# Optimization experiments

Measured on AMD Instinct MI355X. Metric: run time of the kernel, lower is better.

## Reference

```python
import jax, jax.numpy as jnp
import numpy as np

N_SRNA = 20000
N_MRNA = 100000
HID = 128
E_S2M = 1_000_000
E_M2M = 2_000_000
E_LBL = 500_000
N_LAYERS = 2


def setup_inputs() -> dict:
    key = jax.random.key(0)
    ks = jax.random.split(key, 20)
    s = 0.05
    inp = {
        # edge lists (rev edge types are flips, derived inside reference)
        "s2m_src": jax.random.randint(ks[0], (E_S2M,), 0, N_SRNA),
        "s2m_dst": jax.random.randint(ks[1], (E_S2M,), 0, N_MRNA),
        "m2m_src": jax.random.randint(ks[2], (E_M2M,), 0, N_MRNA),
        "m2m_dst": jax.random.randint(ks[3], (E_M2M,), 0, N_MRNA),
        "label_src": jax.random.randint(ks[4], (E_LBL,), 0, N_SRNA),
        "label_dst": jax.random.randint(ks[5], (E_LBL,), 0, N_MRNA),
        # embeddings (node_id is arange over all nodes -> identity lookup)
        "srna_emb": jax.random.normal(ks[6], (N_SRNA, HID), jnp.float32),
        "mrna_emb": jax.random.normal(ks[7], (N_MRNA, HID), jnp.float32),
        # per-layer stacked params. SAGEConv: out = lin_l(mean_agg)+lin_r(x_dst)
        "sage_s2m_Wl": jax.random.normal(ks[8], (N_LAYERS, HID, HID), jnp.float32) * s,
        "sage_s2m_bl": jnp.zeros((N_LAYERS, HID), jnp.float32),
        "sage_s2m_Wr": jax.random.normal(ks[9], (N_LAYERS, HID, HID), jnp.float32) * s,
        "sage_rev_Wl": jax.random.normal(ks[10], (N_LAYERS, HID, HID), jnp.float32) * s,
        "sage_rev_bl": jnp.zeros((N_LAYERS, HID), jnp.float32),
        "sage_rev_Wr": jax.random.normal(ks[11], (N_LAYERS, HID, HID), jnp.float32) * s,
        # GCNConv: out = propagate(norm, x @ W) + b
        "gcn_m2m_W": jax.random.normal(ks[12], (N_LAYERS, HID, HID), jnp.float32) * s,
        "gcn_m2m_b": jnp.zeros((N_LAYERS, HID), jnp.float32),
        "gcn_rev_W": jax.random.normal(ks[13], (N_LAYERS, HID, HID), jnp.float32) * s,
        "gcn_rev_b": jnp.zeros((N_LAYERS, HID), jnp.float32),
    }
    return inp


def _sage(x_src, x_dst, src, dst, n_dst, Wl, bl, Wr):
    # PyG SAGEConv (aggr='mean', root_weight=True): lin_l(mean_msg) + lin_r(x_dst)
    agg = jax.ops.segment_sum(x_src[src], dst, num_segments=n_dst)  # [n_dst, h]
    cnt = jax.ops.segment_sum(jnp.ones((src.shape[0],), x_src.dtype), dst,
                              num_segments=n_dst)
    agg = agg / jnp.maximum(cnt, 1.0)[:, None]
    return agg @ Wl + bl + x_dst @ Wr


def _gcn(x, src, dst, n, W, b):
    # PyG GCNConv: add self-loops, sym-normalize, x @ W, propagate, + bias
    xw = x @ W  # [n, h]
    deg = jax.ops.segment_sum(jnp.ones((src.shape[0],), x.dtype), dst,
                              num_segments=n) + 1.0  # +1 self-loop
    dinv = jax.lax.rsqrt(deg)
    norm = dinv[src] * dinv[dst]  # [E]
    out = jax.ops.segment_sum(norm[:, None] * xw[src], dst, num_segments=n)
    out = out + (dinv * dinv)[:, None] * xw  # self-loop term
    return out + b


def reference(s2m_src, s2m_dst, m2m_src, m2m_dst, label_src, label_dst,
              srna_emb, mrna_emb,
              sage_s2m_Wl, sage_s2m_bl, sage_s2m_Wr,
              sage_rev_Wl, sage_rev_bl, sage_rev_Wr,
              gcn_m2m_W, gcn_m2m_b, gcn_rev_W, gcn_rev_b):
    x_s, x_m = srna_emb, mrna_emb
    for l in range(N_LAYERS):
        # HeteroConv aggr='sum' over edge types per dst node type
        m_new = _sage(x_s, x_m, s2m_src, s2m_dst, N_MRNA,
                      sage_s2m_Wl[l], sage_s2m_bl[l], sage_s2m_Wr[l])
        m_new = m_new + _gcn(x_m, m2m_src, m2m_dst, N_MRNA,
                             gcn_m2m_W[l], gcn_m2m_b[l])
        m_new = m_new + _gcn(x_m, m2m_dst, m2m_src, N_MRNA,
                             gcn_rev_W[l], gcn_rev_b[l])  # rev_similar = flip
        s_new = _sage(x_m, x_s, s2m_dst, s2m_src, N_SRNA,
                      sage_rev_Wl[l], sage_rev_bl[l], sage_rev_Wr[l])
        x_s, x_m = jax.nn.relu(s_new), jax.nn.relu(m_new)
    # Classifier: dot product over labeled (srna, mrna) pairs
    return (x_s[label_src] * x_m[label_dst]).sum(axis=-1)
```

## Files before the change

### kernel.cpp

```cpp
#include <hip/hip_runtime.h>
#include <hip/hip_fp16.h>

#define NS 20000
#define NM 100000
#define H  128
#define ES 1000000
#define EM 2000000
#define EL 500000

#define SH_M 7
#define SH_S 6
#define NB_SD 782
#define NB_SS 313
#define NB_MD 782
#define NB_MS 782
#define CAP_SD 1664
#define CAP_SS 3904
#define CAP_MD 3200
#define CAP_MS 3200
#define MAXCAP 3904
#define CHUNK 4096
#define B_SD ((ES + CHUNK - 1) / CHUNK)
#define B_SS ((ES + CHUNK - 1) / CHUNK)
#define B_MD ((EM + CHUNK - 1) / CHUNK)
#define B_MS ((EM + CHUNK - 1) / CHUNK)
#define VAL_MASK 0x1FFFF

typedef _Float16 half8 __attribute__((ext_vector_type(8)));
typedef float floatx4 __attribute__((ext_vector_type(4)));

__global__ __launch_bounds__(256) void place1_sorted(
        const int* __restrict__ s2m_src, const int* __restrict__ s2m_dst,
        const int* __restrict__ m2m_src, const int* __restrict__ m2m_dst,
        int* __restrict__ bc,
        unsigned int* __restrict__ p_sd, unsigned int* __restrict__ p_ss,
        unsigned int* __restrict__ p_md, unsigned int* __restrict__ p_ms) {
    __shared__ unsigned int rec[CHUNK];
    __shared__ unsigned short eb[CHUNK];
    __shared__ int cnt[1024];
    __shared__ int gbase[1024];

    int b = blockIdx.x;
    const int *keys, *vals; int shift, cap, E, bcoff; unsigned int* pp;
    int cb;
    if (b < B_SD)                    { cb = b;                      keys = s2m_dst; vals = s2m_src; shift = SH_M; cap = CAP_SD; E = ES; bcoff = 0;     pp = p_sd; }
    else if (b < B_SD+B_SS)          { cb = b - B_SD;               keys = s2m_src; vals = s2m_dst; shift = SH_S; cap = CAP_SS; E = ES; bcoff = 16384; pp = p_ss; }
    else if (b < B_SD+B_SS+B_MD)     { cb = b - B_SD - B_SS;        keys = m2m_dst; vals = m2m_src; shift = SH_M; cap = CAP_MD; E = EM; bcoff = 32768; pp = p_md; }
    else                             { cb = b - B_SD - B_SS - B_MD; keys = m2m_src; vals = m2m_dst; shift = SH_M; cap = CAP_MS; E = EM; bcoff = 49152; pp = p_ms; }
    int* bcp = bc + bcoff;

    int t = threadIdx.x;
    int e0 = cb * CHUNK;
    int nv = E - e0; if (nv > CHUNK) nv = CHUNK;

    for (int i = t; i < nv; i += 256) {
        int k = keys[e0 + i];
        int v = vals[e0 + i];
        int bkt = k >> shift;
        rec[i] = ((unsigned int)(k - (bkt << shift)) << 17) | (unsigned int)v;
        eb[i] = (unsigned short)bkt;
    }
#pragma unroll
    for (int j = 0; j < 4; ++j) cnt[t * 4 + j] = 0;
    __syncthreads();
    for (int i = t; i < nv; i += 256) atomicAdd(&cnt[eb[i]], 1);
    __syncthreads();
#pragma unroll
    for (int j = 0; j < 4; ++j) {
        int bk = t * 4 + j;
        int c = cnt[bk];
        if (c > 0) {
            gbase[bk] = atomicAdd(&bcp[bk << 4], c);
            cnt[bk] = 0;
        }
    }
    __syncthreads();
    for (int i = t; i < nv; i += 256) {
        int bk = eb[i];
        int pos = atomicAdd(&cnt[bk], 1);
        int o = gbase[bk] + pos;
        if (o < cap) pp[(size_t)bk * cap + o] = rec[i];
    }
}

__global__ __launch_bounds__(256) void place2_fused(
        const int* __restrict__ bc,
        const unsigned int* __restrict__ p_sd, const unsigned int* __restrict__ p_ss,
        const unsigned int* __restrict__ p_md, const unsigned int* __restrict__ p_ms,
        int* __restrict__ adj_sd, int* __restrict__ adj_ss,
        int* __restrict__ adj_md, int* __restrict__ adj_ms,
        int* __restrict__ off_sd, int* __restrict__ off_ss,
        int* __restrict__ off_md, int* __restrict__ off_ms,
        int* __restrict__ cnt_sd, int* __restrict__ cnt_ss,
        int* __restrict__ cnt_md, int* __restrict__ cnt_ms) {
    __shared__ unsigned int lp[MAXCAP];
    __shared__ int hist[128], cur[128], sbuf[128];
    int b = blockIdx.x;
    int c, lb;
    if (b < NB_SD)                    { c = 0; lb = b; }
    else if (b < NB_SD+NB_SS)         { c = 1; lb = b - NB_SD; }
    else if (b < NB_SD+NB_SS+NB_MD)   { c = 2; lb = b - NB_SD - NB_SS; }
    else                              { c = 3; lb = b - NB_SD - NB_SS - NB_MD; }
    const unsigned int* pp; int *adj, *offp, *cntp; int shift, cap, n;
    switch (c) {
    case 0:  pp = p_sd; adj = adj_sd; offp = off_sd; cntp = cnt_sd; shift = SH_M; cap = CAP_SD; n = NM; break;
    case 1:  pp = p_ss; adj = adj_ss; offp = off_ss; cntp = cnt_ss; shift = SH_S; cap = CAP_SS; n = NS; break;
    case 2:  pp = p_md; adj = adj_md; offp = off_md; cntp = cnt_md; shift = SH_M; cap = CAP_MD; n = NM; break;
    default: pp = p_ms; adj = adj_ms; offp = off_ms; cntp = cnt_ms; shift = SH_M; cap = CAP_MS; n = NM; break;
    }
    int t = threadIdx.x;
    int k = bc[c * 16384 + (lb << 4)];
    if (k > cap) k = cap;
    int base = lb << shift;
    int npb = 1 << shift;
    int bb = lb * cap;
    for (int i = t; i < k; i += 256) lp[i] = pp[(size_t)lb * cap + i];
    if (t < npb) hist[t] = 0;
    __syncthreads();
    for (int i = t; i < k; i += 256) atomicAdd(&hist[lp[i] >> 17], 1);
    __syncthreads();
    int v = (t < npb) ? hist[t] : 0;
    if (t < 128) sbuf[t] = v;
    __syncthreads();
    for (int d = 1; d < 128; d <<= 1) {
        int x = 0;
        if (t >= d && t < 128) x = sbuf[t - d];
        __syncthreads();
        if (t >= d && t < 128) sbuf[t] += x;
        __syncthreads();
    }
    if (t < npb) {
        int excl = sbuf[t] - v;
        cur[t] = excl;
        int node = base + t;
        if (node < n) { offp[node] = bb + excl; cntp[node] = v; }
    }
    __syncthreads();
    for (int i = t; i < k; i += 256) {
        unsigned int p = lp[i];
        int pos = atomicAdd(&cur[p >> 17], 1);
        adj[(size_t)bb + pos] = (int)(p & VAL_MASK);
    }
}

__global__ void finalize_scales(const int* __restrict__ c_md, const int* __restrict__ c_ms,
                                float* __restrict__ dvf, float* __restrict__ dvr) {
    int i = blockIdx.x * blockDim.x + threadIdx.x;
    if (i < NM) {
        dvf[i] = rsqrtf((float)c_md[i] + 1.0f);
        dvr[i] = rsqrtf((float)c_ms[i] + 1.0f);
    }
}

__global__ void to_half(const float* __restrict__ in, __half* __restrict__ out,
                        long long n4) {
    long long i = (long long)blockIdx.x * blockDim.x + threadIdx.x;
    if (i >= n4) return;
    float4 v = *(const float4*)&in[i * 4];
    __half2 h0 = __floats2half2_rn(v.x, v.y);
    __half2 h1 = __floats2half2_rn(v.z, v.w);
    __half2* o = (__half2*)&out[i * 4];
    o[0] = h0; o[1] = h1;
}

__global__ void prep_w(const float* __restrict__ w0, const float* __restrict__ w1,
                       const float* __restrict__ w2, const float* __restrict__ w3,
                       const float* __restrict__ w4, const float* __restrict__ w5,
                       __half* __restrict__ out) {
    int idx = blockIdx.x * 256 + threadIdx.x;
    if (idx >= 12 * H * H) return;
    int mat = idx / (H * H);
    int rem = idx % (H * H);
    int n = rem / H;
    int k = rem % H;
    const float* base;
    switch (mat >> 1) {
    case 0: base = w0; break; case 1: base = w1; break; case 2: base = w2; break;
    case 3: base = w3; break; case 4: base = w4; break; default: base = w5; break;
    }
    base += (size_t)(mat & 1) * H * H;
    out[(size_t)mat * H * H + (size_t)n * H + k] = __float2half(base[(size_t)k * H + n]);
}

__device__ __forceinline__ float4 ldh4(const __half* __restrict__ X, long long idx) {
    float2 raw = *(const float2*)(X + idx);
    __half2 h0 = *(__half2*)&raw.x;
    __half2 h1 = *(__half2*)&raw.y;
    float2 fa = __half22float2(h0);
    float2 fb = __half22float2(h1);
    return make_float4(fa.x, fa.y, fb.x, fb.y);
}

__device__ __forceinline__ void gacc_plain(const __half* __restrict__ X,
                                           const int* __restrict__ adj,
                                           int o, int k, int c, float (&acc)[8]) {
    int j = 0;
    for (; j + 8 <= k; j += 8) {
        int s0 = adj[o+j+0], s1 = adj[o+j+1], s2 = adj[o+j+2], s3 = adj[o+j+3];
        int s4 = adj[o+j+4], s5 = adj[o+j+5], s6 = adj[o+j+6], s7 = adj[o+j+7];
        half8 v0 = *(const half8*)(X + (size_t)s0 * H + c);
        half8 v1 = *(const half8*)(X + (size_t)s1 * H + c);
        half8 v2 = *(const half8*)(X + (size_t)s2 * H + c);
        half8 v3 = *(const half8*)(X + (size_t)s3 * H + c);
        half8 v4 = *(const half8*)(X + (size_t)s4 * H + c);
        half8 v5 = *(const half8*)(X + (size_t)s5 * H + c);
        half8 v6 = *(const half8*)(X + (size_t)s6 * H + c);
        half8 v7 = *(const half8*)(X + (size_t)s7 * H + c);
#pragma unroll
        for (int i = 0; i < 8; ++i)
            acc[i] += (float)v0[i] + (float)v1[i] + (float)v2[i] + (float)v3[i]
                    + (float)v4[i] + (float)v5[i] + (float)v6[i] + (float)v7[i];
    }
    for (; j + 4 <= k; j += 4) {
        int s0 = adj[o+j+0], s1 = adj[o+j+1], s2 = adj[o+j+2], s3 = adj[o+j+3];
        half8 v0 = *(const half8*)(X + (size_t)s0 * H + c);
        half8 v1 = *(const half8*)(X + (size_t)s1 * H + c);
        half8 v2 = *(const half8*)(X + (size_t)s2 * H + c);
        half8 v3 = *(const half8*)(X + (size_t)s3 * H + c);
#pragma unroll
        for (int i = 0; i < 8; ++i)
            acc[i] += (float)v0[i] + (float)v1[i] + (float)v2[i] + (float)v3[i];
    }
    for (; j < k; ++j) {
        int s = adj[o + j];
        half8 v = *(const half8*)(X + (size_t)s * H + c);
#pragma unroll
        for (int i = 0; i < 8; ++i) acc[i] += (float)v[i];
    }
}

__device__ __forceinline__ void gacc_weighted(const __half* __restrict__ X,
                                              const int* __restrict__ adj,
                                              const float* __restrict__ dinv,
                                              int o, int k, int c, float (&acc)[8]) {
    int j = 0;
    for (; j + 8 <= k; j += 8) {
        int s0 = adj[o+j+0], s1 = adj[o+j+1], s2 = adj[o+j+2], s3 = adj[o+j+3];
        int s4 = adj[o+j+4], s5 = adj[o+j+5], s6 = adj[o+j+6], s7 = adj[o+j+7];
        float d0 = dinv[s0], d1 = dinv[s1], d2 = dinv[s2], d3 = dinv[s3];
        float d4 = dinv[s4], d5 = dinv[s5], d6 = dinv[s6], d7 = dinv[s7];
        half8 v0 = *(const half8*)(X + (size_t)s0 * H + c);
        half8 v1 = *(const half8*)(X + (size_t)s1 * H + c);
        half8 v2 = *(const half8*)(X + (size_t)s2 * H + c);
        half8 v3 = *(const half8*)(X + (size_t)s3 * H + c);
        half8 v4 = *(const half8*)(X + (size_t)s4 * H + c);
        half8 v5 = *(const half8*)(X + (size_t)s5 * H + c);
        half8 v6 = *(const half8*)(X + (size_t)s6 * H + c);
        half8 v7 = *(const half8*)(X + (size_t)s7 * H + c);
#pragma unroll
        for (int i = 0; i < 8; ++i)
            acc[i] += d0 * (float)v0[i] + d1 * (float)v1[i] + d2 * (float)v2[i] + d3 * (float)v3[i]
                    + d4 * (float)v4[i] + d5 * (float)v5[i] + d6 * (float)v6[i] + d7 * (float)v7[i];
    }
    for (; j + 4 <= k; j += 4) {
        int s0 = adj[o+j+0], s1 = adj[o+j+1], s2 = adj[o+j+2], s3 = adj[o+j+3];
        float d0 = dinv[s0], d1 = dinv[s1], d2 = dinv[s2], d3 = dinv[s3];
        half8 v0 = *(const half8*)(X + (size_t)s0 * H + c);
        half8 v1 = *(const half8*)(X + (size_t)s1 * H + c);
        half8 v2 = *(const half8*)(X + (size_t)s2 * H + c);
        half8 v3 = *(const half8*)(X + (size_t)s3 * H + c);
#pragma unroll
        for (int i = 0; i < 8; ++i)
            acc[i] += d0 * (float)v0[i] + d1 * (float)v1[i] + d2 * (float)v2[i] + d3 * (float)v3[i];
    }
    for (; j < k; ++j) {
        int s = adj[o + j];
        float ds = dinv[s];
        half8 v = *(const half8*)(X + (size_t)s * H + c);
#pragma unroll
        for (int i = 0; i < 8; ++i) acc[i] += ds * (float)v[i];
    }
}

__device__ __forceinline__ void sth8(__half* __restrict__ X, size_t idx, const float (&a)[8]) {
    half8 h;
#pragma unroll
    for (int i = 0; i < 8; ++i) h[i] = (_Float16)a[i];
    *(half8*)(X + idx) = h;
}

__global__ void mega_gather(const __half* __restrict__ xs16, const __half* __restrict__ xm16,
                            const int* __restrict__ off_sd, const int* __restrict__ cnt_sd,
                            const int* __restrict__ adj_sd,
                            const int* __restrict__ off_md, const int* __restrict__ cnt_md,
                            const int* __restrict__ adj_md,
                            const int* __restrict__ off_ms, const int* __restrict__ cnt_ms,
                            const int* __restrict__ adj_ms,
                            const int* __restrict__ off_ss, const int* __restrict__ cnt_ss,
                            const int* __restrict__ adj_ss,
                            const float* __restrict__ dvf, const float* __restrict__ dvr,
                            __half* __restrict__ SA, __half* __restrict__ Qf,
                            __half* __restrict__ Qr, __half* __restrict__ Qs) {
    long long gid = (long long)blockIdx.x * blockDim.x + threadIdx.x;
    int g = (int)(gid >> 4);
    int c = ((int)gid & 15) * 8;
    float acc[8] = {0.f, 0.f, 0.f, 0.f, 0.f, 0.f, 0.f, 0.f};
    if (g < NM) {
        int k = cnt_sd[g];
        gacc_plain(xs16, adj_sd, off_sd[g], k, c, acc);
        float ic = 1.0f / fmaxf((float)k, 1.0f);
#pragma unroll
        for (int i = 0; i < 8; ++i) acc[i] *= ic;
        sth8(SA, (size_t)g * H + c, acc);
    } else if (g < 2 * NM) {
        int r = g - NM;
        gacc_weighted(xm16, adj_md, dvf, off_md[r], cnt_md[r], c, acc);
        float dd = dvf[r];
        float s2 = dd * dd;
        half8 self = *(const half8*)(xm16 + (size_t)r * H + c);
#pragma unroll
        for (int i = 0; i < 8; ++i) acc[i] = dd * acc[i] + s2 * (float)self[i];
        sth8(Qf, (size_t)r * H + c, acc);
    } else if (g < 3 * NM) {
        int r = g - 2 * NM;
        gacc_weighted(xm16, adj_ms, dvr, off_ms[r], cnt_ms[r], c, acc);
        float dd = dvr[r];
        float s2 = dd * dd;
        half8 self = *(const half8*)(xm16 + (size_t)r * H + c);
#pragma unroll
        for (int i = 0; i < 8; ++i) acc[i] = dd * acc[i] + s2 * (float)self[i];
        sth8(Qr, (size_t)r * H + c, acc);
    } else if (g < 3 * NM + NS) {
        int r = g - 3 * NM;
        int k = cnt_ss[r];
        gacc_plain(xm16, adj_ss, off_ss[r], k, c, acc);
        float ic = 1.0f / fmaxf((float)k, 1.0f);
#pragma unroll
        for (int i = 0; i < 8; ++i) acc[i] *= ic;
        sth8(Qs, (size_t)r * H + c, acc);
    }
}

__device__ __forceinline__ void mfma_stage(const __half* __restrict__ A,
                                           const __half* __restrict__ Wt,
                                           int gr, int M, int nlo, int quad,
                                           floatx4 (&acc)[8]) {
#pragma unroll
    for (int k0 = 0; k0 < 128; k0 += 32) {
        half8 a;
        if (gr < M) {
            a = *(const half8*)(A + (size_t)gr * H + k0 + quad * 8);
        } else {
            float4 z = make_float4(0.f, 0.f, 0.f, 0.f);
            a = *(half8*)&z;
        }
#pragma unroll
        for (int t = 0; t < 8; ++t) {
            half8 b = *(const half8*)(Wt + (size_t)(t * 16 + nlo) * H + k0 + quad * 8);
            acc[t] = __builtin_amdgcn_mfma_f32_16x16x32_f16(a, b, acc[t], 0, 0, 0);
        }
    }
}

__global__ __launch_bounds__(256) void mega_gemm_mfma(
        const __half* __restrict__ SA, const __half* __restrict__ Qf,
        const __half* __restrict__ Qr, const __half* __restrict__ xm_in,
        const __half* __restrict__ Qs, const __half* __restrict__ xs_in,
        const __half* __restrict__ wbuf,
        const float* __restrict__ bl, const float* __restrict__ gb,
        const float* __restrict__ grb, const float* __restrict__ bls,
        __half* __restrict__ xm_out, __half* __restrict__ xs_out,
        int MBLK, int layer)
{
    const int tid = threadIdx.x;
    const int w = tid >> 6;
    const int lane = tid & 63;
    const int quad = lane >> 4;
    const int nlo = lane & 15;
    const size_t HH = (size_t)H * H;

    floatx4 acc[8];
#pragma unroll
    for (int t = 0; t < 8; ++t) {
        acc[t][0] = 0.f; acc[t][1] = 0.f; acc[t][2] = 0.f; acc[t][3] = 0.f;
    }

    if ((int)blockIdx.x < MBLK) {
        const int bm = blockIdx.x * 64 + w * 16;
        const int gr = bm + nlo;
        mfma_stage(SA,    wbuf + (0 * 2 + layer) * HH, gr, NM, nlo, quad, acc);
        mfma_stage(xm_in, wbuf + (1 * 2 + layer) * HH, gr, NM, nlo, quad, acc);
        mfma_stage(Qf,    wbuf + (2 * 2 + layer) * HH, gr, NM, nlo, quad, acc);
        mfma_stage(Qr,    wbuf + (3 * 2 + layer) * HH, gr, NM, nlo, quad, acc);
#pragma unroll
        for (int t = 0; t < 8; ++t) {
            int col = t * 16 + nlo;
            float bias = bl[col] + gb[col] + grb[col];
#pragma unroll
            for (int i = 0; i < 4; ++i) {
                int r = bm + quad * 4 + i;
                if (r < NM)
                    xm_out[(size_t)r * H + col] = __float2half(fmaxf(acc[t][i] + bias, 0.f));
            }
        }
    } else {
        const int bm = ((int)blockIdx.x - MBLK) * 64 + w * 16;
        const int gr = bm + nlo;
        mfma_stage(Qs,    wbuf + (4 * 2 + layer) * HH, gr, NS, nlo, quad, acc);
        mfma_stage(xs_in, wbuf + (5 * 2 + layer) * HH, gr, NS, nlo, quad, acc);
#pragma unroll
        for (int t = 0; t < 8; ++t) {
            int col = t * 16 + nlo;
            float bias = bls[col];
#pragma unroll
            for (int i = 0; i < 4; ++i) {
                int r = bm + quad * 4 + i;
                if (r < NS)
                    xs_out[(size_t)r * H + col] = __float2half(fmaxf(acc[t][i] + bias, 0.f));
            }
        }
    }
}

__global__ void classify(const __half* __restrict__ xs16, const __half* __restrict__ xm16,
                         const int* __restrict__ ls, const int* __restrict__ ld,
                         float* __restrict__ out, int P) {
    long long gid = (long long)blockIdx.x * blockDim.x + threadIdx.x;
    int p = (int)(gid >> 5);
    if (p >= P) return;
    int lane = (int)gid & 31;
    int a = ls[p], b = ld[p];
    float4 u = ldh4(xs16, (long long)a * H + lane * 4);
    float4 v = ldh4(xm16, (long long)b * H + lane * 4);
    float s = u.x * v.x + u.y * v.y + u.z * v.z + u.w * v.w;
    for (int off = 16; off > 0; off >>= 1) s += __shfl_down(s, off, 32);
    if (lane == 0) out[p] = s;
}

extern "C" void kernel_launch(void* const* d_in, const int* in_sizes, int n_in,
                              void* d_out, int out_size, void* d_ws, size_t ws_size,
                              hipStream_t stream) {
    const int* s2m_src = (const int*)d_in[0];
    const int* s2m_dst = (const int*)d_in[1];
    const int* m2m_src = (const int*)d_in[2];
    const int* m2m_dst = (const int*)d_in[3];
    const int* lbl_src = (const int*)d_in[4];
    const int* lbl_dst = (const int*)d_in[5];
    const float* s_emb = (const float*)d_in[6];
    const float* m_emb = (const float*)d_in[7];
    const float* Wl_s2m = (const float*)d_in[8];
    const float* bl_s2m = (const float*)d_in[9];
    const float* Wr_s2m = (const float*)d_in[10];
    const float* Wl_rev = (const float*)d_in[11];
    const float* bl_rev = (const float*)d_in[12];
    const float* Wr_rev = (const float*)d_in[13];
    const float* gW  = (const float*)d_in[14];
    const float* gb  = (const float*)d_in[15];
    const float* grW = (const float*)d_in[16];
    const float* grb = (const float*)d_in[17];

    __half* hws = (__half*)d_ws;
    size_t ho = 0;
    __half* xm16_a = hws + ho; ho += (size_t)NM * H;
    __half* xm16_b = hws + ho; ho += (size_t)NM * H;
    __half* xs16_a = hws + ho; ho += (size_t)NS * H;
    __half* xs16_b = hws + ho; ho += (size_t)NS * H;
    __half* SA = hws + ho; ho += (size_t)NM * H;
    __half* Qf = hws + ho; ho += (size_t)NM * H;
    __half* Qr = hws + ho; ho += (size_t)NM * H;
    __half* Qs = hws + ho; ho += (size_t)NS * H;
    __half* wbuf = hws + ho; ho += (size_t)12 * H * H;

    float* fws = (float*)(hws + ho);
    size_t fo = 0;
    float* dvf = fws + fo; fo += NM;
    float* dvr = fws + fo; fo += NM;

    int* ip = (int*)(fws + fo);
    size_t io = 0;
    int* off_sd = ip + io; io += NM;
    int* off_ss = ip + io; io += NS;
    int* off_md = ip + io; io += NM;
    int* off_ms = ip + io; io += NM;
    int* cnt_sd = ip + io; io += NM;
    int* cnt_ss = ip + io; io += NS;
    int* cnt_md = ip + io; io += NM;
    int* cnt_ms = ip + io; io += NM;
    int* bc     = ip + io; io += 4 * 16384;
    int* adj_sd = ip + io; io += NB_SD * CAP_SD;
    int* adj_ss = ip + io; io += NB_SS * CAP_SS;
    int* adj_md = ip + io; io += NB_MD * CAP_MD;
    int* adj_ms = ip + io; io += NB_MS * CAP_MS;

    unsigned int* p_sd = (unsigned int*)SA;
    unsigned int* p_ss = p_sd + (size_t)NB_SD * CAP_SD;
    unsigned int* p_md = p_ss + (size_t)NB_SS * CAP_SS;
    unsigned int* p_ms = p_md + (size_t)NB_MD * CAP_MD;

    const int bM = (NM + 255) / 256;

    hipMemsetAsync(bc, 0, 4 * 16384 * sizeof(int), stream);
    place1_sorted<<<B_SD + B_SS + B_MD + B_MS, 256, 0, stream>>>(
        s2m_src, s2m_dst, m2m_src, m2m_dst, bc, p_sd, p_ss, p_md, p_ms);
    place2_fused<<<NB_SD + NB_SS + NB_MD + NB_MS, 256, 0, stream>>>(
        bc, p_sd, p_ss, p_md, p_ms,
        adj_sd, adj_ss, adj_md, adj_ms,
        off_sd, off_ss, off_md, off_ms,
        cnt_sd, cnt_ss, cnt_md, cnt_ms);
    finalize_scales<<<bM, 256, 0, stream>>>(cnt_md, cnt_ms, dvf, dvr);

    const long long n4m = (long long)NM * H / 4;
    const long long n4s = (long long)NS * H / 4;
    to_half<<<(int)((n4m + 255) / 256), 256, 0, stream>>>(m_emb, xm16_a, n4m);
    to_half<<<(int)((n4s + 255) / 256), 256, 0, stream>>>(s_emb, xs16_a, n4s);
    prep_w<<<(12 * H * H + 255) / 256, 256, 0, stream>>>(
        Wl_s2m, Wr_s2m, gW, grW, Wl_rev, Wr_rev, wbuf);

    const int gMega = (int)(((long long)(3 * NM + NS) * 16 + 255) / 256);
    const int MBLK = (NM + 63) / 64;
    const int SBLK = (NS + 63) / 64;

    const __half* xin_m = xm16_a;
    const __half* xin_s = xs16_a;
    __half* xout_m = xm16_b;
    __half* xout_s = xs16_b;

    for (int l = 0; l < 2; ++l) {
        const size_t bo = (size_t)l * H;

        mega_gather<<<gMega, 256, 0, stream>>>(xin_s, xin_m,
                                               off_sd, cnt_sd, adj_sd,
                                               off_md, cnt_md, adj_md,
                                               off_ms, cnt_ms, adj_ms,
                                               off_ss, cnt_ss, adj_ss,
                                               dvf, dvr, SA, Qf, Qr, Qs);

        mega_gemm_mfma<<<MBLK + SBLK, 256, 0, stream>>>(
            SA, Qf, Qr, xin_m, Qs, xin_s, wbuf,
            bl_s2m + bo, gb + bo, grb + bo, bl_rev + bo,
            xout_m, xout_s, MBLK, l);

        const __half* tm = xin_m; xin_m = xout_m; xout_m = (__half*)tm;
        const __half* ts = xin_s; xin_s = xout_s; xout_s = (__half*)ts;
    }

    classify<<<(int)(((long long)EL * 32 + 255) / 256), 256, 0, stream>>>(
        xin_s, xin_m, lbl_src, lbl_dst, (float*)d_out, EL);
}
```

Measured before the change: 961.1 us.

## Sort gather nodes by degree bin into worklists to balance wavefront work

Place2 now builds a histogram of per-node degree bins (groups of 8 neighbors), a small scan kernel turns it into descending-degree bin offsets, and the finalize kernel scatters node ids into per-relation worklists ordered by degree. The mega_gather kernel reads node ids from these worklists, so nodes with similar degrees share wavefronts and divergence on the neighbor loop shrinks. The cost is an extra tiny kernel, extra atomics, and an indirection per node, and output writes to SA/Q buffers become scattered rather than contiguous.

```diff
diff --git a/kernel.cpp b/kernel.cpp
--- a/kernel.cpp
+++ b/kernel.cpp
@@ -92,9 +92,11 @@
         int* __restrict__ off_sd, int* __restrict__ off_ss,
         int* __restrict__ off_md, int* __restrict__ off_ms,
         int* __restrict__ cnt_sd, int* __restrict__ cnt_ss,
-        int* __restrict__ cnt_md, int* __restrict__ cnt_ms) {
+        int* __restrict__ cnt_md, int* __restrict__ cnt_ms,
+        int* __restrict__ binCnt) {
     __shared__ unsigned int lp[MAXCAP];
     __shared__ int hist[128], cur[128], sbuf[128];
+    __shared__ int lbin[64];
     int b = blockIdx.x;
     int c, lb;
     if (b < NB_SD)                    { c = 0; lb = b; }
@@ -116,6 +118,7 @@
     int bb = lb * cap;
     for (int i = t; i < k; i += 256) lp[i] = pp[(size_t)lb * cap + i];
     if (t < npb) hist[t] = 0;
+    if (t < 64) lbin[t] = 0;
     __syncthreads();
     for (int i = t; i < k; i += 256) atomicAdd(&hist[lp[i] >> 17], 1);
     __syncthreads();
@@ -133,9 +136,14 @@
         int excl = sbuf[t] - v;
         cur[t] = excl;
         int node = base + t;
-        if (node < n) { offp[node] = bb + excl; cntp[node] = v; }
-    }
-    __syncthreads();
+        if (node < n) {
+            offp[node] = bb + excl; cntp[node] = v;
+            int bin = (v + 7) >> 3; if (bin > 63) bin = 63;
+            atomicAdd(&lbin[bin], 1);
+        }
+    }
+    __syncthreads();
+    if (t < 64 && lbin[t] > 0) atomicAdd(&binCnt[c * 64 + t], lbin[t]);
     for (int i = t; i < k; i += 256) {
         unsigned int p = lp[i];
         int pos = atomicAdd(&cur[p >> 17], 1);
@@ -143,13 +151,53 @@
     }
 }
 
-__global__ void finalize_scales(const int* __restrict__ c_md, const int* __restrict__ c_ms,
-                                float* __restrict__ dvf, float* __restrict__ dvr) {
-    int i = blockIdx.x * blockDim.x + threadIdx.x;
-    if (i < NM) {
-        dvf[i] = rsqrtf((float)c_md[i] + 1.0f);
-        dvr[i] = rsqrtf((float)c_ms[i] + 1.0f);
-    }
+__global__ void bin_scan(const int* __restrict__ binCnt, int* __restrict__ binBase) {
+    int t = threadIdx.x;
+    int s = t >> 6, b = t & 63;
+    int off = 0;
+    for (int b2 = 63; b2 > b; --b2) off += binCnt[s * 64 + b2];
+    binBase[t] = off;
+}
+
+__global__ __launch_bounds__(256) void finalize_scatter(
+        const int* __restrict__ c_sd, const int* __restrict__ c_ss,
+        const int* __restrict__ c_md, const int* __restrict__ c_ms,
+        float* __restrict__ dvf, float* __restrict__ dvr,
+        int* __restrict__ binBase,
+        int* __restrict__ wl_sd, int* __restrict__ wl_ss,
+        int* __restrict__ wl_md, int* __restrict__ wl_ms) {
+    __shared__ int lc[256], lb[256];
+    int t = threadIdx.x;
+    int i = blockIdx.x * 256 + t;
+    lc[t] = 0;
+    __syncthreads();
+    int b_sd = 0, p_sd = 0, b_md = 0, p_md = 0, b_ms = 0, p_ms = 0, b_ss = 0, p_ss = 0;
+    bool vm = i < NM, vs = i < NS;
+    if (vm) {
+        int km = c_md[i], kr = c_ms[i], ks = c_sd[i];
+        dvf[i] = rsqrtf((float)km + 1.0f);
+        dvr[i] = rsqrtf((float)kr + 1.0f);
+        b_sd = (ks + 7) >> 3; if (b_sd > 63) b_sd = 63;
+        b_md = (km + 7) >> 3; if (b_md > 63) b_md = 63;
+        b_ms = (kr + 7) >> 3; if (b_ms > 63) b_ms = 63;
+        p_sd = atomicAdd(&lc[0 * 64 + b_sd], 1);
+        p_md = atomicAdd(&lc[2 * 64 + b_md], 1);
+        p_ms = atomicAdd(&lc[3 * 64 + b_ms], 1);
+    }
+    if (vs) {
+        int kq = c_ss[i];
+        b_ss = (kq + 7) >> 3; if (b_ss > 63) b_ss = 63;
+        p_ss = atomicAdd(&lc[1 * 64 + b_ss], 1);
+    }
+    __syncthreads();
+    if (lc[t] > 0) lb[t] = atomicAdd(&binBase[t], lc[t]);
+    __syncthreads();
+    if (vm) {
+        wl_sd[lb[0 * 64 + b_sd] + p_sd] = i;
+        wl_md[lb[2 * 64 + b_md] + p_md] = i;
+        wl_ms[lb[3 * 64 + b_ms] + p_ms] = i;
+    }
+    if (vs) wl_ss[lb[1 * 64 + b_ss] + p_ss] = i;
 }
 
 __global__ void to_half(const float* __restrict__ in, __half* __restrict__ out,
@@ -288,6 +336,8 @@
                             const int* __restrict__ adj_ms,
                             const int* __restrict__ off_ss, const int* __restrict__ cnt_ss,
                             const int* __restrict__ adj_ss,
+                            const int* __restrict__ wl_sd, const int* __restrict__ wl_md,
+                            const int* __restrict__ wl_ms, const int* __restrict__ wl_ss,
                             const float* __restrict__ dvf, const float* __restrict__ dvr,
                             __half* __restrict__ SA, __half* __restrict__ Qf,
                             __half* __restrict__ Qr, __half* __restrict__ Qs) {
@@ -296,14 +346,15 @@
     int c = ((int)gid & 15) * 8;
     float acc[8] = {0.f, 0.f, 0.f, 0.f, 0.f, 0.f, 0.f, 0.f};
     if (g < NM) {
-        int k = cnt_sd[g];
-        gacc_plain(xs16, adj_sd, off_sd[g], k, c, acc);
+        int r = wl_sd[g];
+        int k = cnt_sd[r];
+        gacc_plain(xs16, adj_sd, off_sd[r], k, c, acc);
         float ic = 1.0f / fmaxf((float)k, 1.0f);
 #pragma unroll
         for (int i = 0; i < 8; ++i) acc[i] *= ic;
-        sth8(SA, (size_t)g * H + c, acc);
+        sth8(SA, (size_t)r * H + c, acc);
     } else if (g < 2 * NM) {
-        int r = g - NM;
+        int r = wl_md[g - NM];
         gacc_weighted(xm16, adj_md, dvf, off_md[r], cnt_md[r], c, acc);
         float dd = dvf[r];
         float s2 = dd * dd;
@@ -312,7 +363,7 @@
         for (int i = 0; i < 8; ++i) acc[i] = dd * acc[i] + s2 * (float)self[i];
         sth8(Qf, (size_t)r * H + c, acc);
     } else if (g < 3 * NM) {
-        int r = g - 2 * NM;
+        int r = wl_ms[g - 2 * NM];
         gacc_weighted(xm16, adj_ms, dvr, off_ms[r], cnt_ms[r], c, acc);
         float dd = dvr[r];
         float s2 = dd * dd;
@@ -321,7 +372,7 @@
         for (int i = 0; i < 8; ++i) acc[i] = dd * acc[i] + s2 * (float)self[i];
         sth8(Qr, (size_t)r * H + c, acc);
     } else if (g < 3 * NM + NS) {
-        int r = g - 3 * NM;
+        int r = wl_ss[g - 3 * NM];
         int k = cnt_ss[r];
         gacc_plain(xm16, adj_ss, off_ss[r], k, c, acc);
         float ic = 1.0f / fmaxf((float)k, 1.0f);
@@ -477,6 +528,12 @@
     int* cnt_md = ip + io; io += NM;
     int* cnt_ms = ip + io; io += NM;
     int* bc     = ip + io; io += 4 * 16384;
+    int* binCnt  = ip + io; io += 256;
+    int* binBase = ip + io; io += 256;
+    int* wl_sd  = ip + io; io += NM;
+    int* wl_ss  = ip + io; io += NS;
+    int* wl_md  = ip + io; io += NM;
+    int* wl_ms  = ip + io; io += NM;
     int* adj_sd = ip + io; io += NB_SD * CAP_SD;
     int* adj_ss = ip + io; io += NB_SS * CAP_SS;
     int* adj_md = ip + io; io += NB_MD * CAP_MD;
@@ -489,15 +546,18 @@
 
     const int bM = (NM + 255) / 256;
 
-    hipMemsetAsync(bc, 0, 4 * 16384 * sizeof(int), stream);
+    hipMemsetAsync(bc, 0, (4 * 16384 + 256) * sizeof(int), stream);
     place1_sorted<<<B_SD + B_SS + B_MD + B_MS, 256, 0, stream>>>(
         s2m_src, s2m_dst, m2m_src, m2m_dst, bc, p_sd, p_ss, p_md, p_ms);
     place2_fused<<<NB_SD + NB_SS + NB_MD + NB_MS, 256, 0, stream>>>(
         bc, p_sd, p_ss, p_md, p_ms,
         adj_sd, adj_ss, adj_md, adj_ms,
         off_sd, off_ss, off_md, off_ms,
-        cnt_sd, cnt_ss, cnt_md, cnt_ms);
-    finalize_scales<<<bM, 256, 0, stream>>>(cnt_md, cnt_ms, dvf, dvr);
+        cnt_sd, cnt_ss, cnt_md, cnt_ms, binCnt);
+    bin_scan<<<1, 256, 0, stream>>>(binCnt, binBase);
+    finalize_scatter<<<bM, 256, 0, stream>>>(
+        cnt_sd, cnt_ss, cnt_md, cnt_ms, dvf, dvr, binBase,
+        wl_sd, wl_ss, wl_md, wl_ms);
 
     const long long n4m = (long long)NM * H / 4;
     const long long n4s = (long long)NS * H / 4;
@@ -523,6 +583,7 @@
                                                off_md, cnt_md, adj_md,
                                                off_ms, cnt_ms, adj_ms,
                                                off_ss, cnt_ss, adj_ss,
+                                               wl_sd, wl_md, wl_ms, wl_ss,
                                                dvf, dvr, SA, Qf, Qr, Qs);
 
         mega_gemm_mfma<<<MBLK + SBLK, 256, 0, stream>>>(
```

Result: slower. 989.6 us (+3.0%).

## Store node features in column-sliced layout so gathers touch 32-byte slices

Applied to the files above, without the earlier changes.

Feature matrices are re-laid out as 8 column slices of 16 halves each ([slice][row][16]) instead of row-major, and the gather kernel assigns each block one slice so that concurrently running blocks gather from a smaller working set that fits better in cache. The fp16 conversion, GEMM A-loads and output stores, and the classifier are all updated to read and write this layout. The cost is 32-byte random accesses per neighbor instead of full 256-byte rows, and the adjacency and dinv indices are reread once for each of the 8 slices.

```diff
diff --git a/kernel.cpp b/kernel.cpp
--- a/kernel.cpp
+++ b/kernel.cpp
@@ -25,6 +25,12 @@
 #define B_MD ((EM + CHUNK - 1) / CHUNK)
 #define B_MS ((EM + CHUNK - 1) / CHUNK)
 #define VAL_MASK 0x1FFFF
+
+#define RB_SD ((NM + 127) / 128)
+#define RB_MD ((NM + 127) / 128)
+#define RB_MS ((NM + 127) / 128)
+#define RB_SS ((NS + 127) / 128)
+#define RB_TOT (RB_SD + RB_MD + RB_MS + RB_SS)
 
 typedef _Float16 half8 __attribute__((ext_vector_type(8)));
 typedef float floatx4 __attribute__((ext_vector_type(4)));
@@ -152,15 +158,28 @@
     }
 }
 
-__global__ void to_half(const float* __restrict__ in, __half* __restrict__ out,
-                        long long n4) {
-    long long i = (long long)blockIdx.x * blockDim.x + threadIdx.x;
-    if (i >= n4) return;
-    float4 v = *(const float4*)&in[i * 4];
-    __half2 h0 = __floats2half2_rn(v.x, v.y);
-    __half2 h1 = __floats2half2_rn(v.z, v.w);
-    __half2* o = (__half2*)&out[i * 4];
-    o[0] = h0; o[1] = h1;
+__global__ __launch_bounds__(256) void to_half_blocked(const float* __restrict__ in,
+                                                       __half* __restrict__ out, int N) {
+    __shared__ __half tile[128 * 136];
+    int rb = blockIdx.x, t = threadIdx.x;
+    int r0 = rb * 128;
+    int nr = N - r0; if (nr > 128) nr = 128;
+    for (int i = t; i < nr * 32; i += 256) {
+        int row = i >> 5, c4 = (i & 31) << 2;
+        float4 v = *(const float4*)&in[(size_t)(r0 + row) * H + c4];
+        __half2 h0 = __floats2half2_rn(v.x, v.y);
+        __half2 h1 = __floats2half2_rn(v.z, v.w);
+        __half2* p = (__half2*)&tile[row * 136 + c4];
+        p[0] = h0; p[1] = h1;
+    }
+    __syncthreads();
+    for (int cidx = t; cidx < 2048; cidx += 256) {
+        int slice = cidx >> 8, rem = cidx & 255, row = rem >> 1, lh8 = (rem & 1) << 3;
+        if (row < nr) {
+            half8 v = *(half8*)&tile[row * 136 + slice * 16 + lh8];
+            *(half8*)(out + (((size_t)slice * N + r0 + row) << 4) + lh8) = v;
+        }
+    }
 }
 
 __global__ void prep_w(const float* __restrict__ w0, const float* __restrict__ w1,
@@ -182,30 +201,21 @@
     out[(size_t)mat * H * H + (size_t)n * H + k] = __float2half(base[(size_t)k * H + n]);
 }
 
-__device__ __forceinline__ float4 ldh4(const __half* __restrict__ X, long long idx) {
-    float2 raw = *(const float2*)(X + idx);
-    __half2 h0 = *(__half2*)&raw.x;
-    __half2 h1 = *(__half2*)&raw.y;
-    float2 fa = __half22float2(h0);
-    float2 fb = __half22float2(h1);
-    return make_float4(fa.x, fa.y, fb.x, fb.y);
-}
-
-__device__ __forceinline__ void gacc_plain(const __half* __restrict__ X,
-                                           const int* __restrict__ adj,
-                                           int o, int k, int c, float (&acc)[8]) {
+__device__ __forceinline__ void gaccb_plain(const __half* __restrict__ X,
+                                            const int* __restrict__ adj,
+                                            int o, int k, size_t sb, int lh8, float (&acc)[8]) {
     int j = 0;
     for (; j + 8 <= k; j += 8) {
         int s0 = adj[o+j+0], s1 = adj[o+j+1], s2 = adj[o+j+2], s3 = adj[o+j+3];
         int s4 = adj[o+j+4], s5 = adj[o+j+5], s6 = adj[o+j+6], s7 = adj[o+j+7];
-        half8 v0 = *(const half8*)(X + (size_t)s0 * H + c);
-        half8 v1 = *(const half8*)(X + (size_t)s1 * H + c);
-        half8 v2 = *(const half8*)(X + (size_t)s2 * H + c);
-        half8 v3 = *(const half8*)(X + (size_t)s3 * H + c);
-        half8 v4 = *(const half8*)(X + (size_t)s4 * H + c);
-        half8 v5 = *(const half8*)(X + (size_t)s5 * H + c);
-        half8 v6 = *(const half8*)(X + (size_t)s6 * H + c);
-        half8 v7 = *(const half8*)(X + (size_t)s7 * H + c);
+        half8 v0 = *(const half8*)(X + ((sb + s0) << 4) + lh8);
+        half8 v1 = *(const half8*)(X + ((sb + s1) << 4) + lh8);
+        half8 v2 = *(const half8*)(X + ((sb + s2) << 4) + lh8);
+        half8 v3 = *(const half8*)(X + ((sb + s3) << 4) + lh8);
+        half8 v4 = *(const half8*)(X + ((sb + s4) << 4) + lh8);
+        half8 v5 = *(const half8*)(X + ((sb + s5) << 4) + lh8);
+        half8 v6 = *(const half8*)(X + ((sb + s6) << 4) + lh8);
+        half8 v7 = *(const half8*)(X + ((sb + s7) << 4) + lh8);
 #pragma unroll
         for (int i = 0; i < 8; ++i)
             acc[i] += (float)v0[i] + (float)v1[i] + (float)v2[i] + (float)v3[i]
@@ -213,40 +223,40 @@
     }
     for (; j + 4 <= k; j += 4) {
         int s0 = adj[o+j+0], s1 = adj[o+j+1], s2 = adj[o+j+2], s3 = adj[o+j+3];
-        half8 v0 = *(const half8*)(X + (size_t)s0 * H + c);
-        half8 v1 = *(const half8*)(X + (size_t)s1 * H + c);
-        half8 v2 = *(const half8*)(X + (size_t)s2 * H + c);
-        half8 v3 = *(const half8*)(X + (size_t)s3 * H + c);
+        half8 v0 = *(const half8*)(X + ((sb + s0) << 4) + lh8);
+        half8 v1 = *(const half8*)(X + ((sb + s1) << 4) + lh8);
+        half8 v2 = *(const half8*)(X + ((sb + s2) << 4) + lh8);
+        half8 v3 = *(const half8*)(X + ((sb + s3) << 4) + lh8);
 #pragma unroll
         for (int i = 0; i < 8; ++i)
             acc[i] += (float)v0[i] + (float)v1[i] + (float)v2[i] + (float)v3[i];
     }
     for (; j < k; ++j) {
         int s = adj[o + j];
-        half8 v = *(const half8*)(X + (size_t)s * H + c);
+        half8 v = *(const half8*)(X + ((sb + s) << 4) + lh8);
 #pragma unroll
         for (int i = 0; i < 8; ++i) acc[i] += (float)v[i];
     }
 }
 
-__device__ __forceinline__ void gacc_weighted(const __half* __restrict__ X,
-                                              const int* __restrict__ adj,
-                                              const float* __restrict__ dinv,
-                                              int o, int k, int c, float (&acc)[8]) {
+__device__ __forceinline__ void gaccb_weighted(const __half* __restrict__ X,
+                                               const int* __restrict__ adj,
+                                               const float* __restrict__ dinv,
+                                               int o, int k, size_t sb, int lh8, float (&acc)[8]) {
     int j = 0;
     for (; j + 8 <= k; j += 8) {
         int s0 = adj[o+j+0], s1 = adj[o+j+1], s2 = adj[o+j+2], s3 = adj[o+j+3];
         int s4 = adj[o+j+4], s5 = adj[o+j+5], s6 = adj[o+j+6], s7 = adj[o+j+7];
         float d0 = dinv[s0], d1 = dinv[s1], d2 = dinv[s2], d3 = dinv[s3];
         float d4 = dinv[s4], d5 = dinv[s5], d6 = dinv[s6], d7 = dinv[s7];
-        half8 v0 = *(const half8*)(X + (size_t)s0 * H + c);
-        half8 v1 = *(const half8*)(X + (size_t)s1 * H + c);
-        half8 v2 = *(const half8*)(X + (size_t)s2 * H + c);
-        half8 v3 = *(const half8*)(X + (size_t)s3 * H + c);
-        half8 v4 = *(const half8*)(X + (size_t)s4 * H + c);
-        half8 v5 = *(const half8*)(X + (size_t)s5 * H + c);
-        half8 v6 = *(const half8*)(X + (size_t)s6 * H + c);
-        half8 v7 = *(const half8*)(X + (size_t)s7 * H + c);
+        half8 v0 = *(const half8*)(X + ((sb + s0) << 4) + lh8);
+        half8 v1 = *(const half8*)(X + ((sb + s1) << 4) + lh8);
+        half8 v2 = *(const half8*)(X + ((sb + s2) << 4) + lh8);
+        half8 v3 = *(const half8*)(X + ((sb + s3) << 4) + lh8);
+        half8 v4 = *(const half8*)(X + ((sb + s4) << 4) + lh8);
+        half8 v5 = *(const half8*)(X + ((sb + s5) << 4) + lh8);
+        half8 v6 = *(const half8*)(X + ((sb + s6) << 4) + lh8);
+        half8 v7 = *(const half8*)(X + ((sb + s7) << 4) + lh8);
 #pragma unroll
         for (int i = 0; i < 8; ++i)
             acc[i] += d0 * (float)v0[i] + d1 * (float)v1[i] + d2 * (float)v2[i] + d3 * (float)v3[i]
@@ -255,10 +265,10 @@
     for (; j + 4 <= k; j += 4) {
         int s0 = adj[o+j+0], s1 = adj[o+j+1], s2 = adj[o+j+2], s3 = adj[o+j+3];
         float d0 = dinv[s0], d1 = dinv[s1], d2 = dinv[s2], d3 = dinv[s3];
-        half8 v0 = *(const half8*)(X + (size_t)s0 * H + c);
-        half8 v1 = *(const half8*)(X + (size_t)s1 * H + c);
-        half8 v2 = *(const half8*)(X + (size_t)s2 * H + c);
-        half8 v3 = *(const half8*)(X + (size_t)s3 * H + c);
+        half8 v0 = *(const half8*)(X + ((sb + s0) << 4) + lh8);
+        half8 v1 = *(const half8*)(X + ((sb + s1) << 4) + lh8);
+        half8 v2 = *(const half8*)(X + ((sb + s2) << 4) + lh8);
+        half8 v3 = *(const half8*)(X + ((sb + s3) << 4) + lh8);
 #pragma unroll
         for (int i = 0; i < 8; ++i)
             acc[i] += d0 * (float)v0[i] + d1 * (float)v1[i] + d2 * (float)v2[i] + d3 * (float)v3[i];
@@ -266,68 +276,81 @@
     for (; j < k; ++j) {
         int s = adj[o + j];
         float ds = dinv[s];
-        half8 v = *(const half8*)(X + (size_t)s * H + c);
+        half8 v = *(const half8*)(X + ((sb + s) << 4) + lh8);
 #pragma unroll
         for (int i = 0; i < 8; ++i) acc[i] += ds * (float)v[i];
     }
 }
 
-__device__ __forceinline__ void sth8(__half* __restrict__ X, size_t idx, const float (&a)[8]) {
+__device__ __forceinline__ void sth8p(__half* __restrict__ p, const float (&a)[8]) {
     half8 h;
 #pragma unroll
     for (int i = 0; i < 8; ++i) h[i] = (_Float16)a[i];
-    *(half8*)(X + idx) = h;
-}
-
-__global__ void mega_gather(const __half* __restrict__ xs16, const __half* __restrict__ xm16,
-                            const int* __restrict__ off_sd, const int* __restrict__ cnt_sd,
-                            const int* __restrict__ adj_sd,
-                            const int* __restrict__ off_md, const int* __restrict__ cnt_md,
-                            const int* __restrict__ adj_md,
-                            const int* __restrict__ off_ms, const int* __restrict__ cnt_ms,
-                            const int* __restrict__ adj_ms,
-                            const int* __restrict__ off_ss, const int* __restrict__ cnt_ss,
-                            const int* __restrict__ adj_ss,
-                            const float* __restrict__ dvf, const float* __restrict__ dvr,
-                            __half* __restrict__ SA, __half* __restrict__ Qf,
-                            __half* __restrict__ Qr, __half* __restrict__ Qs) {
-    long long gid = (long long)blockIdx.x * blockDim.x + threadIdx.x;
-    int g = (int)(gid >> 4);
-    int c = ((int)gid & 15) * 8;
+    *(half8*)p = h;
+}
+
+__global__ __launch_bounds__(256) void mega_gather(
+        const __half* __restrict__ xsb, const __half* __restrict__ xmb,
+        const int* __restrict__ off_sd, const int* __restrict__ cnt_sd,
+        const int* __restrict__ adj_sd,
+        const int* __restrict__ off_md, const int* __restrict__ cnt_md,
+        const int* __restrict__ adj_md,
+        const int* __restrict__ off_ms, const int* __restrict__ cnt_ms,
+        const int* __restrict__ adj_ms,
+        const int* __restrict__ off_ss, const int* __restrict__ cnt_ss,
+        const int* __restrict__ adj_ss,
+        const float* __restrict__ dvf, const float* __restrict__ dvr,
+        __half* __restrict__ SA, __half* __restrict__ Qf,
+        __half* __restrict__ Qr, __half* __restrict__ Qs) {
+    int slice = blockIdx.x & 7;
+    int rb = (int)blockIdx.x >> 3;
+    int t = threadIdx.x;
+    int task = t >> 1;
+    int lh8 = (t & 1) << 3;
     float acc[8] = {0.f, 0.f, 0.f, 0.f, 0.f, 0.f, 0.f, 0.f};
-    if (g < NM) {
-        int k = cnt_sd[g];
-        gacc_plain(xs16, adj_sd, off_sd[g], k, c, acc);
+
+    if (rb < RB_SD) {
+        int r = rb * 128 + task;
+        if (r >= NM) return;
+        int k = cnt_sd[r];
+        size_t sb = (size_t)slice * NS;
+        gaccb_plain(xsb, adj_sd, off_sd[r], k, sb, lh8, acc);
         float ic = 1.0f / fmaxf((float)k, 1.0f);
 #pragma unroll
         for (int i = 0; i < 8; ++i) acc[i] *= ic;
-        sth8(SA, (size_t)g * H + c, acc);
-    } else if (g < 2 * NM) {
-        int r = g - NM;
-        gacc_weighted(xm16, adj_md, dvf, off_md[r], cnt_md[r], c, acc);
+        sth8p(SA + (((size_t)slice * NM + r) << 4) + lh8, acc);
+    } else if (rb < RB_SD + RB_MD) {
+        int r = (rb - RB_SD) * 128 + task;
+        if (r >= NM) return;
+        size_t sb = (size_t)slice * NM;
+        gaccb_weighted(xmb, adj_md, dvf, off_md[r], cnt_md[r], sb, lh8, acc);
         float dd = dvf[r];
         float s2 = dd * dd;
-        half8 self = *(const half8*)(xm16 + (size_t)r * H + c);
+        half8 self = *(const half8*)(xmb + ((sb + r) << 4) + lh8);
 #pragma unroll
         for (int i = 0; i < 8; ++i) acc[i] = dd * acc[i] + s2 * (float)self[i];
-        sth8(Qf, (size_t)r * H + c, acc);
-    } else if (g < 3 * NM) {
-        int r = g - 2 * NM;
-        gacc_weighted(xm16, adj_ms, dvr, off_ms[r], cnt_ms[r], c, acc);
+        sth8p(Qf + (((size_t)slice * NM + r) << 4) + lh8, acc);
+    } else if (rb < RB_SD + RB_MD + RB_MS) {
+        int r = (rb - RB_SD - RB_MD) * 128 + task;
+        if (r >= NM) return;
+        size_t sb = (size_t)slice * NM;
+        gaccb_weighted(xmb, adj_ms, dvr, off_ms[r], cnt_ms[r], sb, lh8, acc);
         float dd = dvr[r];
         float s2 = dd * dd;
-        half8 self = *(const half8*)(xm16 + (size_t)r * H + c);
+        half8 self = *(const half8*)(xmb + ((sb + r) << 4) + lh8);
 #pragma unroll
         for (int i = 0; i < 8; ++i) acc[i] = dd * acc[i] + s2 * (float)self[i];
-        sth8(Qr, (size_t)r * H + c, acc);
-    } else if (g < 3 * NM + NS) {
-        int r = g - 3 * NM;
+        sth8p(Qr + (((size_t)slice * NM + r) << 4) + lh8, acc);
+    } else {
+        int r = (rb - RB_SD - RB_MD - RB_MS) * 128 + task;
+        if (r >= NS) return;
         int k = cnt_ss[r];
-        gacc_plain(xm16, adj_ss, off_ss[r], k, c, acc);
+        size_t sb = (size_t)slice * NM;
+        gaccb_plain(xmb, adj_ss, off_ss[r], k, sb, lh8, acc);
         float ic = 1.0f / fmaxf((float)k, 1.0f);
 #pragma unroll
         for (int i = 0; i < 8; ++i) acc[i] *= ic;
-        sth8(Qs, (size_t)r * H + c, acc);
+        sth8p(Qs + (((size_t)slice * NS + r) << 4) + lh8, acc);
     }
 }
 
@@ -337,9 +360,10 @@
                                            floatx4 (&acc)[8]) {
 #pragma unroll
     for (int k0 = 0; k0 < 128; k0 += 32) {
+        int col = k0 + quad * 8;
         half8 a;
         if (gr < M) {
-            a = *(const half8*)(A + (size_t)gr * H + k0 + quad * 8);
+            a = *(const half8*)(A + (((size_t)(col >> 4) * M + gr) << 4) + (col & 15));
         } else {
             float4 z = make_float4(0.f, 0.f, 0.f, 0.f);
             a = *(half8*)&z;
@@ -390,7 +414,8 @@
             for (int i = 0; i < 4; ++i) {
                 int r = bm + quad * 4 + i;
                 if (r < NM)
-                    xm_out[(size_t)r * H + col] = __float2half(fmaxf(acc[t][i] + bias, 0.f));
+                    xm_out[(((size_t)t * NM + r) << 4) + nlo] =
+                        __float2half(fmaxf(acc[t][i] + bias, 0.f));
             }
         }
     } else {
@@ -406,10 +431,20 @@
             for (int i = 0; i < 4; ++i) {
                 int r = bm + quad * 4 + i;
                 if (r < NS)
-                    xs_out[(size_t)r * H + col] = __float2half(fmaxf(acc[t][i] + bias, 0.f));
+                    xs_out[(((size_t)t * NS + r) << 4) + nlo] =
+                        __float2half(fmaxf(acc[t][i] + bias, 0.f));
             }
         }
     }
+}
+
+__device__ __forceinline__ float4 ldh4p(const __half* __restrict__ p) {
+    float2 raw = *(const float2*)p;
+    __half2 h0 = *(__half2*)&raw.x;
+    __half2 h1 = *(__half2*)&raw.y;
+    float2 fa = __half22float2(h0);
+    float2 fb = __half22float2(h1);
+    return make_float4(fa.x, fa.y, fb.x, fb.y);
 }
 
 __global__ void classify(const __half* __restrict__ xs16, const __half* __restrict__ xm16,
@@ -420,8 +455,9 @@
     if (p >= P) return;
     int lane = (int)gid & 31;
     int a = ls[p], b = ld[p];
-    float4 u = ldh4(xs16, (long long)a * H + lane * 4);
-    float4 v = ldh4(xm16, (long long)b * H + lane * 4);
+    int sl = lane >> 2, w4 = (lane & 3) << 2;
+    float4 u = ldh4p(xs16 + (((size_t)sl * NS + a) << 4) + w4);
+    float4 v = ldh4p(xm16 + (((size_t)sl * NM + b) << 4) + w4);
     float s = u.x * v.x + u.y * v.y + u.z * v.z + u.w * v.w;
     for (int off = 16; off > 0; off >>= 1) s += __shfl_down(s, off, 32);
     if (lane == 0) out[p] = s;
@@ -499,14 +535,11 @@
         cnt_sd, cnt_ss, cnt_md, cnt_ms);
     finalize_scales<<<bM, 256, 0, stream>>>(cnt_md, cnt_ms, dvf, dvr);
 
-    const long long n4m = (long long)NM * H / 4;
-    const long long n4s = (long long)NS * H / 4;
-    to_half<<<(int)((n4m + 255) / 256), 256, 0, stream>>>(m_emb, xm16_a, n4m);
-    to_half<<<(int)((n4s + 255) / 256), 256, 0, stream>>>(s_emb, xs16_a, n4s);
+    to_half_blocked<<<(NM + 127) / 128, 256, 0, stream>>>(m_emb, xm16_a, NM);
+    to_half_blocked<<<(NS + 127) / 128, 256, 0, stream>>>(s_emb, xs16_a, NS);
     prep_w<<<(12 * H * H + 255) / 256, 256, 0, stream>>>(
         Wl_s2m, Wr_s2m, gW, grW, Wl_rev, Wr_rev, wbuf);
 
-    const int gMega = (int)(((long long)(3 * NM + NS) * 16 + 255) / 256);
     const int MBLK = (NM + 63) / 64;
     const int SBLK = (NS + 63) / 64;
 
@@ -518,12 +551,12 @@
     for (int l = 0; l < 2; ++l) {
         const size_t bo = (size_t)l * H;
 
-        mega_gather<<<gMega, 256, 0, stream>>>(xin_s, xin_m,
-                                               off_sd, cnt_sd, adj_sd,
-                                               off_md, cnt_md, adj_md,
-                                               off_ms, cnt_ms, adj_ms,
-                                               off_ss, cnt_ss, adj_ss,
-                                               dvf, dvr, SA, Qf, Qr, Qs);
+        mega_gather<<<RB_TOT * 8, 256, 0, stream>>>(xin_s, xin_m,
+                                                    off_sd, cnt_sd, adj_sd,
+                                                    off_md, cnt_md, adj_md,
+                                                    off_ms, cnt_ms, adj_ms,
+                                                    off_ss, cnt_ss, adj_ss,
+                                                    dvf, dvr, SA, Qf, Qr, Qs);
 
         mega_gemm_mfma<<<MBLK + SBLK, 256, 0, stream>>>(
             SA, Qf, Qr, xin_m, Qs, xin_s, wbuf,
```

Measured after the change: 1.406 ms. 1.46x slower.
